# Performance work log

Measured on AMD Instinct MI355X. Metric: run time of the kernel, lower is better.

Reference implementation:

```python
import jax, jax.numpy as jnp
import numpy as np

B, S, N, C, OUT = 16, 1024, 4096, 768, 256


def setup_inputs() -> dict:
    key = jax.random.key(0)
    k0, k1, k2, k3, k4 = jax.random.split(key, 5)
    seed_xyz = jax.random.normal(k0, (B, S, 3), jnp.float32)   # normalized seed coords
    p_last = jax.random.normal(k1, (B, N, 3), jnp.float32)     # lift3d last-stage coords
    f_last = jax.random.normal(k2, (B, C, N), jnp.float32)     # lift3d last-stage features (channel-first)
    W = jax.random.normal(k3, (OUT, C), jnp.float32) * 0.02    # Conv1d(C, 256, kernel_size=1) weight
    b = jax.random.normal(k4, (OUT,), jnp.float32) * 0.02      # Conv1d bias
    return {"seed_xyz": seed_xyz, "p_last": p_last, "f_last": f_last, "W": W, "b": b}


def reference(seed_xyz, p_last, f_last, W, b):
    # Squared pairwise distances [B,S,N] (argmin invariant to sqrt)
    d2 = (jnp.sum(seed_xyz * seed_xyz, axis=-1, keepdims=True)          # [B,S,1]
          - 2.0 * jnp.einsum('bsd,bnd->bsn', seed_xyz, p_last)          # [B,S,N]
          + jnp.sum(p_last * p_last, axis=-1)[:, None, :])              # [B,1,N]
    idx = jnp.argmin(d2, axis=-1)                                       # [B,S]
    # Gather nearest-neighbor features: [B,C,N] -> [B,C,S]
    gathered = jnp.take_along_axis(f_last, idx[:, None, :], axis=2)
    # 1x1 Conv1d projector: [B,C,S] x [OUT,C] -> [B,OUT,S]
    seed_features = jnp.einsum('bcs,oc->bos', gathered, W) + b[None, :, None]
    return seed_features
```

## Files before the change

### kernel.cpp

```cpp
#include <hip/hip_runtime.h>
#include <stdint.h>

#define B_   16
#define S_   1024
#define N_   4096
#define C_   768
#define OUT_ 256

typedef short bf16x8 __attribute__((ext_vector_type(8)));
typedef short bf16x4 __attribute__((ext_vector_type(4)));
typedef float f32x4  __attribute__((ext_vector_type(4)));

#define GLOBAL_AS __attribute__((address_space(1)))
#define LDS_AS    __attribute__((address_space(3)))

__device__ __forceinline__ unsigned short f2bf(float f) {
    unsigned int u = __float_as_uint(f);
    u += 0x7fffu + ((u >> 16) & 1u);
    return (unsigned short)(u >> 16);
}

__device__ __forceinline__ void gl_lds16(const void* gsrc, void* ldst) {
    __builtin_amdgcn_global_load_lds((const GLOBAL_AS void*)gsrc,
                                     (LDS_AS void*)ldst, 16, 0, 0);
}

__global__ __launch_bounds__(256) void k_wconv(const float* __restrict__ W,
                                               unsigned short* __restrict__ Wb) {
    int i = blockIdx.x * 256 + threadIdx.x;
    Wb[i] = f2bf(W[i]);
}

__global__ __launch_bounds__(256) void k_argmin(const float* __restrict__ seed,
                                                const float* __restrict__ pl,
                                                int* __restrict__ idx_out) {
    const int t    = threadIdx.x;
    const int lane = t & 63;
    const int w    = t >> 6;
    const int gw   = blockIdx.x * 4 + w;
    const int b    = gw >> 8;
    const int s0   = (gw & 255) * 4;

    float sx[4], sy[4], sz[4], s2[4], best[4];
    int   bidx[4];
#pragma unroll
    for (int j = 0; j < 4; ++j) {
        const float* sp = seed + (size_t)(b * S_ + s0 + j) * 3;
        sx[j] = sp[0]; sy[j] = sp[1]; sz[j] = sp[2];
        s2[j] = __fadd_rn(__fadd_rn(__fmul_rn(sx[j], sx[j]),
                                    __fmul_rn(sy[j], sy[j])),
                          __fmul_rn(sz[j], sz[j]));
        best[j] = 3.4e38f;
        bidx[j] = 0;
    }
    const float* pb = pl + (size_t)b * N_ * 3;

    for (int k = 0; k < N_ / 64; ++k) {
        const int   n  = k * 64 + lane;
        const float px = pb[n * 3 + 0];
        const float py = pb[n * 3 + 1];
        const float pz = pb[n * 3 + 2];
        const float p2 = __fadd_rn(__fadd_rn(__fmul_rn(px, px),
                                             __fmul_rn(py, py)),
                                   __fmul_rn(pz, pz));
#pragma unroll
        for (int j = 0; j < 4; ++j) {
            float dot = __fadd_rn(__fadd_rn(__fmul_rn(sx[j], px),
                                            __fmul_rn(sy[j], py)),
                                  __fmul_rn(sz[j], pz));
            float d2  = __fadd_rn(__fsub_rn(s2[j], __fmul_rn(2.0f, dot)), p2);
            if (d2 < best[j]) { best[j] = d2; bidx[j] = n; }
        }
    }

#pragma unroll
    for (int j = 0; j < 4; ++j) {
#pragma unroll
        for (int off = 32; off >= 1; off >>= 1) {
            float ob = __shfl_xor(best[j], off, 64);
            int   oi = __shfl_xor(bidx[j], off, 64);
            bool take = (ob < best[j]) || (ob == best[j] && oi < bidx[j]);
            if (take) { best[j] = ob; bidx[j] = oi; }
        }
        if (lane == 0) idx_out[b * S_ + s0 + j] = bidx[j];
    }
}

__global__ __launch_bounds__(256, 2) void k_pgemm(const float* __restrict__ f,
                                                  const unsigned short* __restrict__ Wb,
                                                  unsigned short* __restrict__ P) {
    __shared__ unsigned short ldsF[128 * 36];
    __shared__ unsigned short ldsW[256 * 32];
    const int t    = threadIdx.x;
    const int b    = blockIdx.x >> 5;
    const int nt   = blockIdx.x & 31;
    const int n0   = nt * 128;
    const int lane = t & 63;
    const int w    = t >> 6;
    const int wm   = w & 1;
    const int wo   = w >> 1;
    const int quad = lane >> 4, l16 = lane & 15;

    f32x4 acc[4][8];
#pragma unroll
    for (int i = 0; i < 4; ++i)
#pragma unroll
        for (int j = 0; j < 8; ++j) acc[i][j] = (f32x4){0.f, 0.f, 0.f, 0.f};

    const int cb = t >> 5;
    const int nb = t & 31;
    const float* fB = f + (size_t)b * C_ * N_ + n0 + nb * 4;
    const unsigned short* wSrc = Wb + (size_t)(t >> 2) * C_ + (t & 3) * 8;

    for (int kt = 0; kt < C_ / 32; ++kt) {
        const int k0 = kt * 32;
#pragma unroll
        for (int i = 0; i < 4; ++i)
            gl_lds16(wSrc + (size_t)i * 64 * C_ + k0, ldsW + i * 2048 + t * 8);
        f32x4 v[4];
#pragma unroll
        for (int j = 0; j < 4; ++j)
            v[j] = *(const f32x4*)(fB + (size_t)(k0 + cb * 4 + j) * N_);
#pragma unroll
        for (int i = 0; i < 4; ++i) {
            bf16x4 pk = {(short)f2bf(v[0][i]), (short)f2bf(v[1][i]),
                         (short)f2bf(v[2][i]), (short)f2bf(v[3][i])};
            *(bf16x4*)(ldsF + (nb * 4 + i) * 36 + cb * 4) = pk;
        }
        __syncthreads();

        bf16x8 aF[4], bF[8];
#pragma unroll
        for (int mi = 0; mi < 4; ++mi) {
            const unsigned short* p = ldsF + (wm * 64 + mi * 16 + l16) * 36 + quad * 8;
            bf16x4 lo = *(const bf16x4*)p;
            bf16x4 hi = *(const bf16x4*)(p + 4);
            aF[mi] = __builtin_shufflevector(lo, hi, 0, 1, 2, 3, 4, 5, 6, 7);
        }
#pragma unroll
        for (int oi = 0; oi < 8; ++oi)
            bF[oi] = *(const bf16x8*)(ldsW + (wo * 128 + oi * 16 + l16) * 32 + quad * 8);
#pragma unroll
        for (int mi = 0; mi < 4; ++mi)
#pragma unroll
            for (int oi = 0; oi < 8; ++oi)
                acc[mi][oi] = __builtin_amdgcn_mfma_f32_16x16x32_bf16(
                    aF[mi], bF[oi], acc[mi][oi], 0, 0, 0);
        __syncthreads();
    }

    unsigned short* Pb = P + ((size_t)b * N_ + n0) * OUT_;
#pragma unroll
    for (int mi = 0; mi < 4; ++mi) {
#pragma unroll
        for (int r = 0; r < 4; ++r) {
            const int n = wm * 64 + mi * 16 + quad * 4 + r;
            unsigned short* row = Pb + (size_t)n * OUT_;
#pragma unroll
            for (int oi = 0; oi < 8; ++oi) {
                const int o = wo * 128 + oi * 16 + l16;
                row[o] = f2bf(acc[mi][oi][r]);
            }
        }
    }
}

__global__ __launch_bounds__(256) void k_out(const unsigned short* __restrict__ P,
                                             const int* __restrict__ idx,
                                             const float* __restrict__ bias,
                                             float* __restrict__ out) {
    __shared__ unsigned short tl[64 * 260];
    const int t  = threadIdx.x;
    const int b  = blockIdx.x >> 4;
    const int st = blockIdx.x & 15;
    const int s0 = st * 64;
    const unsigned short* Pb = P + (size_t)b * N_ * OUT_;

#pragma unroll
    for (int i = 0; i < 8; ++i) {
        const int g = i * 256 + t;
        const int s = g >> 5;
        const int p = g & 31;
        const int n = idx[b * S_ + s0 + s];
        const unsigned short* src = Pb + (size_t)n * OUT_ + p * 8;
        uint2 u0 = *(const uint2*)src;
        uint2 u1 = *(const uint2*)(src + 4);
        *(uint2*)(tl + s * 260 + p * 8)     = u0;
        *(uint2*)(tl + s * 260 + p * 8 + 4) = u1;
    }
    __syncthreads();

    const int lane = t & 63;
    const int w    = t >> 6;
    float* ob = out + (size_t)b * OUT_ * S_ + s0;
#pragma unroll 4
    for (int oo = 0; oo < 64; ++oo) {
        const int o = w * 64 + oo;
        const unsigned short u = tl[lane * 260 + o];
        const float val = __uint_as_float(((unsigned int)u) << 16) + bias[o];
        ob[(size_t)o * S_ + lane] = val;
    }
}

extern "C" void kernel_launch(void* const* d_in, const int* in_sizes, int n_in,
                              void* d_out, int out_size, void* d_ws, size_t ws_size,
                              hipStream_t stream) {
    const float* seed = (const float*)d_in[0];
    const float* pl   = (const float*)d_in[1];
    const float* f    = (const float*)d_in[2];
    const float* W    = (const float*)d_in[3];
    const float* bias = (const float*)d_in[4];
    float* out = (float*)d_out;

    int* idx            = (int*)d_ws;
    unsigned short* Wb  = (unsigned short*)((char*)d_ws + 65536);
    unsigned short* P   = (unsigned short*)((char*)d_ws + 524288);

    k_wconv <<<768,  256, 0, stream>>>(W, Wb);
    k_argmin<<<1024, 256, 0, stream>>>(seed, pl, idx);
    k_pgemm <<<512,  256, 0, stream>>>(f, Wb, P);
    k_out   <<<256,  256, 0, stream>>>(P, idx, bias, out);
}
```

Before: 320.4 us.

## Double-buffer pgemm LDS tiles with register prefetch of next K slice

```diff
diff --git a/kernel.cpp b/kernel.cpp
--- a/kernel.cpp
+++ b/kernel.cpp
@@ -11,18 +11,10 @@
 typedef short bf16x4 __attribute__((ext_vector_type(4)));
 typedef float f32x4  __attribute__((ext_vector_type(4)));
 
-#define GLOBAL_AS __attribute__((address_space(1)))
-#define LDS_AS    __attribute__((address_space(3)))
-
 __device__ __forceinline__ unsigned short f2bf(float f) {
     unsigned int u = __float_as_uint(f);
     u += 0x7fffu + ((u >> 16) & 1u);
     return (unsigned short)(u >> 16);
-}
-
-__device__ __forceinline__ void gl_lds16(const void* gsrc, void* ldst) {
-    __builtin_amdgcn_global_load_lds((const GLOBAL_AS void*)gsrc,
-                                     (LDS_AS void*)ldst, 16, 0, 0);
 }
 
 __global__ __launch_bounds__(256) void k_wconv(const float* __restrict__ W,
@@ -89,8 +81,8 @@
 __global__ __launch_bounds__(256, 2) void k_pgemm(const float* __restrict__ f,
                                                   const unsigned short* __restrict__ Wb,
                                                   unsigned short* __restrict__ P) {
-    __shared__ unsigned short ldsF[128 * 36];
-    __shared__ unsigned short ldsW[256 * 32];
+    __shared__ unsigned short ldsF[2][128 * 36];
+    __shared__ unsigned short ldsW[2][256 * 40];
     const int t    = threadIdx.x;
     const int b    = blockIdx.x >> 5;
     const int nt   = blockIdx.x & 31;
@@ -110,42 +102,77 @@
     const int cb = t >> 5;
     const int nb = t & 31;
     const float* fB = f + (size_t)b * C_ * N_ + n0 + nb * 4;
-    const unsigned short* wSrc = Wb + (size_t)(t >> 2) * C_ + (t & 3) * 8;
-
+    const int wr = t >> 2;
+    const int wc = t & 3;
+    const unsigned short* wSrc = Wb + (size_t)wr * C_ + wc * 8;
+
+    f32x4  v[4];
+    bf16x8 wv[4];
+
+#pragma unroll
+    for (int j = 0; j < 4; ++j)
+        v[j] = *(const f32x4*)(fB + (size_t)(cb * 4 + j) * N_);
+#pragma unroll
+    for (int i = 0; i < 4; ++i)
+        wv[i] = *(const bf16x8*)(wSrc + (size_t)i * 64 * C_);
+#pragma unroll
+    for (int i = 0; i < 4; ++i) {
+        bf16x4 pk = {(short)f2bf(v[0][i]), (short)f2bf(v[1][i]),
+                     (short)f2bf(v[2][i]), (short)f2bf(v[3][i])};
+        *(bf16x4*)(&ldsF[0][(nb * 4 + i) * 36 + cb * 4]) = pk;
+    }
+#pragma unroll
+    for (int i = 0; i < 4; ++i)
+        *(bf16x8*)(&ldsW[0][(wr + i * 64) * 40 + wc * 8]) = wv[i];
+    __syncthreads();
+
+#pragma unroll 2
     for (int kt = 0; kt < C_ / 32; ++kt) {
-        const int k0 = kt * 32;
-#pragma unroll
-        for (int i = 0; i < 4; ++i)
-            gl_lds16(wSrc + (size_t)i * 64 * C_ + k0, ldsW + i * 2048 + t * 8);
-        f32x4 v[4];
-#pragma unroll
-        for (int j = 0; j < 4; ++j)
-            v[j] = *(const f32x4*)(fB + (size_t)(k0 + cb * 4 + j) * N_);
-#pragma unroll
-        for (int i = 0; i < 4; ++i) {
-            bf16x4 pk = {(short)f2bf(v[0][i]), (short)f2bf(v[1][i]),
-                         (short)f2bf(v[2][i]), (short)f2bf(v[3][i])};
-            *(bf16x4*)(ldsF + (nb * 4 + i) * 36 + cb * 4) = pk;
-        }
-        __syncthreads();
+        const int rb = kt & 1;
+        const unsigned short* fR = &ldsF[rb][0];
+        const unsigned short* wR = &ldsW[rb][0];
+        unsigned short* fW = &ldsF[rb ^ 1][0];
+        unsigned short* wW = &ldsW[rb ^ 1][0];
+
+        if (kt < C_ / 32 - 1) {
+            const int k1 = (kt + 1) * 32;
+#pragma unroll
+            for (int j = 0; j < 4; ++j)
+                v[j] = *(const f32x4*)(fB + (size_t)(k1 + cb * 4 + j) * N_);
+#pragma unroll
+            for (int i = 0; i < 4; ++i)
+                wv[i] = *(const bf16x8*)(wSrc + (size_t)i * 64 * C_ + k1);
+        }
 
         bf16x8 aF[4], bF[8];
 #pragma unroll
         for (int mi = 0; mi < 4; ++mi) {
-            const unsigned short* p = ldsF + (wm * 64 + mi * 16 + l16) * 36 + quad * 8;
+            const unsigned short* p = fR + (wm * 64 + mi * 16 + l16) * 36 + quad * 8;
             bf16x4 lo = *(const bf16x4*)p;
             bf16x4 hi = *(const bf16x4*)(p + 4);
             aF[mi] = __builtin_shufflevector(lo, hi, 0, 1, 2, 3, 4, 5, 6, 7);
         }
 #pragma unroll
         for (int oi = 0; oi < 8; ++oi)
-            bF[oi] = *(const bf16x8*)(ldsW + (wo * 128 + oi * 16 + l16) * 32 + quad * 8);
+            bF[oi] = *(const bf16x8*)(wR + (wo * 128 + oi * 16 + l16) * 40 + quad * 8);
 #pragma unroll
         for (int mi = 0; mi < 4; ++mi)
 #pragma unroll
             for (int oi = 0; oi < 8; ++oi)
                 acc[mi][oi] = __builtin_amdgcn_mfma_f32_16x16x32_bf16(
                     aF[mi], bF[oi], acc[mi][oi], 0, 0, 0);
+
+        if (kt < C_ / 32 - 1) {
+#pragma unroll
+            for (int i = 0; i < 4; ++i) {
+                bf16x4 pk = {(short)f2bf(v[0][i]), (short)f2bf(v[1][i]),
+                             (short)f2bf(v[2][i]), (short)f2bf(v[3][i])};
+                *(bf16x4*)(fW + (nb * 4 + i) * 36 + cb * 4) = pk;
+            }
+#pragma unroll
+            for (int i = 0; i < 4; ++i)
+                *(bf16x8*)(wW + (wr + i * 64) * 40 + wc * 8) = wv[i];
+        }
         __syncthreads();
     }
 
```

Result: slower. 328.6 us (+2.6%).

## Halve pgemm N-tile to 64 for more blocks and occupancy; vectorize W conversion

Applied to the files above, without the earlier changes.

```diff
diff --git a/kernel.cpp b/kernel.cpp
--- a/kernel.cpp
+++ b/kernel.cpp
@@ -6,6 +6,7 @@
 #define N_   4096
 #define C_   768
 #define OUT_ 256
+#define NT_  (C_ / 32)
 
 typedef short bf16x8 __attribute__((ext_vector_type(8)));
 typedef short bf16x4 __attribute__((ext_vector_type(4)));
@@ -27,8 +28,14 @@
 
 __global__ __launch_bounds__(256) void k_wconv(const float* __restrict__ W,
                                                unsigned short* __restrict__ Wb) {
-    int i = blockIdx.x * 256 + threadIdx.x;
-    Wb[i] = f2bf(W[i]);
+    int i = (blockIdx.x * 256 + threadIdx.x) * 8;
+    f32x4 a = *(const f32x4*)(W + i);
+    f32x4 c = *(const f32x4*)(W + i + 4);
+    bf16x8 o = {(short)f2bf(a[0]), (short)f2bf(a[1]),
+                (short)f2bf(a[2]), (short)f2bf(a[3]),
+                (short)f2bf(c[0]), (short)f2bf(c[1]),
+                (short)f2bf(c[2]), (short)f2bf(c[3])};
+    *(bf16x8*)(Wb + i) = o;
 }
 
 __global__ __launch_bounds__(256) void k_argmin(const float* __restrict__ seed,
@@ -86,66 +93,61 @@
     }
 }
 
-__global__ __launch_bounds__(256, 2) void k_pgemm(const float* __restrict__ f,
+__global__ __launch_bounds__(256, 4) void k_pgemm(const float* __restrict__ f,
                                                   const unsigned short* __restrict__ Wb,
                                                   unsigned short* __restrict__ P) {
-    __shared__ unsigned short ldsF[128 * 36];
+    __shared__ unsigned short ldsF[64 * 36];
     __shared__ unsigned short ldsW[256 * 32];
     const int t    = threadIdx.x;
-    const int b    = blockIdx.x >> 5;
-    const int nt   = blockIdx.x & 31;
-    const int n0   = nt * 128;
+    const int b    = blockIdx.x >> 6;
+    const int nt   = blockIdx.x & 63;
+    const int n0   = nt * 64;
     const int lane = t & 63;
     const int w    = t >> 6;
-    const int wm   = w & 1;
-    const int wo   = w >> 1;
     const int quad = lane >> 4, l16 = lane & 15;
 
-    f32x4 acc[4][8];
+    f32x4 acc[4][4];
 #pragma unroll
     for (int i = 0; i < 4; ++i)
 #pragma unroll
-        for (int j = 0; j < 8; ++j) acc[i][j] = (f32x4){0.f, 0.f, 0.f, 0.f};
-
-    const int cb = t >> 5;
-    const int nb = t & 31;
+        for (int j = 0; j < 4; ++j) acc[i][j] = (f32x4){0.f, 0.f, 0.f, 0.f};
+
+    const int cb = t >> 4;
+    const int nb = t & 15;
     const float* fB = f + (size_t)b * C_ * N_ + n0 + nb * 4;
     const unsigned short* wSrc = Wb + (size_t)(t >> 2) * C_ + (t & 3) * 8;
 
-    for (int kt = 0; kt < C_ / 32; ++kt) {
+    for (int kt = 0; kt < NT_; ++kt) {
         const int k0 = kt * 32;
 #pragma unroll
         for (int i = 0; i < 4; ++i)
             gl_lds16(wSrc + (size_t)i * 64 * C_ + k0, ldsW + i * 2048 + t * 8);
-        f32x4 v[4];
-#pragma unroll
-        for (int j = 0; j < 4; ++j)
-            v[j] = *(const f32x4*)(fB + (size_t)(k0 + cb * 4 + j) * N_);
+        f32x4 v0 = *(const f32x4*)(fB + (size_t)(k0 + cb * 2 + 0) * N_);
+        f32x4 v1 = *(const f32x4*)(fB + (size_t)(k0 + cb * 2 + 1) * N_);
 #pragma unroll
         for (int i = 0; i < 4; ++i) {
-            bf16x4 pk = {(short)f2bf(v[0][i]), (short)f2bf(v[1][i]),
-                         (short)f2bf(v[2][i]), (short)f2bf(v[3][i])};
-            *(bf16x4*)(ldsF + (nb * 4 + i) * 36 + cb * 4) = pk;
+            unsigned int pk = (unsigned int)f2bf(v0[i]) |
+                              ((unsigned int)f2bf(v1[i]) << 16);
+            *(unsigned int*)(ldsF + (nb * 4 + i) * 36 + cb * 2) = pk;
         }
         __syncthreads();
 
-        bf16x8 aF[4], bF[8];
+        bf16x8 aF[4];
 #pragma unroll
         for (int mi = 0; mi < 4; ++mi) {
-            const unsigned short* p = ldsF + (wm * 64 + mi * 16 + l16) * 36 + quad * 8;
+            const unsigned short* p = ldsF + (mi * 16 + l16) * 36 + quad * 8;
             bf16x4 lo = *(const bf16x4*)p;
             bf16x4 hi = *(const bf16x4*)(p + 4);
             aF[mi] = __builtin_shufflevector(lo, hi, 0, 1, 2, 3, 4, 5, 6, 7);
         }
 #pragma unroll
-        for (int oi = 0; oi < 8; ++oi)
-            bF[oi] = *(const bf16x8*)(ldsW + (wo * 128 + oi * 16 + l16) * 32 + quad * 8);
-#pragma unroll
-        for (int mi = 0; mi < 4; ++mi)
-#pragma unroll
-            for (int oi = 0; oi < 8; ++oi)
+        for (int oi = 0; oi < 4; ++oi) {
+            bf16x8 bF = *(const bf16x8*)(ldsW + (w * 64 + oi * 16 + l16) * 32 + quad * 8);
+#pragma unroll
+            for (int mi = 0; mi < 4; ++mi)
                 acc[mi][oi] = __builtin_amdgcn_mfma_f32_16x16x32_bf16(
-                    aF[mi], bF[oi], acc[mi][oi], 0, 0, 0);
+                    aF[mi], bF, acc[mi][oi], 0, 0, 0);
+        }
         __syncthreads();
     }
 
@@ -154,11 +156,11 @@
     for (int mi = 0; mi < 4; ++mi) {
 #pragma unroll
         for (int r = 0; r < 4; ++r) {
-            const int n = wm * 64 + mi * 16 + quad * 4 + r;
+            const int n = mi * 16 + quad * 4 + r;
             unsigned short* row = Pb + (size_t)n * OUT_;
 #pragma unroll
-            for (int oi = 0; oi < 8; ++oi) {
-                const int o = wo * 128 + oi * 16 + l16;
+            for (int oi = 0; oi < 4; ++oi) {
+                const int o = w * 64 + oi * 16 + l16;
                 row[o] = f2bf(acc[mi][oi][r]);
             }
         }
@@ -216,8 +218,8 @@
     unsigned short* Wb  = (unsigned short*)((char*)d_ws + 65536);
     unsigned short* P   = (unsigned short*)((char*)d_ws + 524288);
 
-    k_wconv <<<768,  256, 0, stream>>>(W, Wb);
+    k_wconv <<<96,   256, 0, stream>>>(W, Wb);
     k_argmin<<<1024, 256, 0, stream>>>(seed, pl, idx);
-    k_pgemm <<<512,  256, 0, stream>>>(f, Wb, P);
+    k_pgemm <<<1024, 256, 0, stream>>>(f, Wb, P);
     k_out   <<<256,  256, 0, stream>>>(P, idx, bias, out);
 }
```

New measurement: 338.1 us. 1.06x slower.
